# Kernel optimization log

Hardware: AMD Instinct MI355X
Metric: run time of the kernel (lower is better)

Reference implementation:

```python
import jax, jax.numpy as jnp
import numpy as np

N_NODES = 100000
N_EDGES = 1600000
IN_DIM = 256
HIDDEN = 128
N_CLASSES = 10


def setup_inputs() -> dict:
    key = jax.random.key(0)
    k1, k2, k3, k4 = jax.random.split(key, 4)
    x = jax.random.normal(k1, (N_NODES, IN_DIM), dtype=jnp.float32)
    edge_index = jax.random.randint(k2, (2, N_EDGES), 0, N_NODES, dtype=jnp.int64)
    # Glorot-ish init for weights
    W1 = jax.random.normal(k3, (IN_DIM, HIDDEN), dtype=jnp.float32) * (1.0 / np.sqrt(IN_DIM))
    b1 = jnp.zeros((HIDDEN,), dtype=jnp.float32)
    W2 = jax.random.normal(k4, (HIDDEN, N_CLASSES), dtype=jnp.float32) * (1.0 / np.sqrt(HIDDEN))
    b2 = jnp.zeros((N_CLASSES,), dtype=jnp.float32)
    return {"x": x, "edge_index": edge_index, "W1": W1, "b1": b1, "W2": W2, "b2": b2}


def _gcn_norm(edge_index, num_nodes):
    # PyG gcn_norm with add_self_loops=False, edge_weight=1:
    # deg over destination (col), norm = d^-1/2[src] * d^-1/2[dst]
    row, col = edge_index[0], edge_index[1]
    deg = jax.ops.segment_sum(jnp.ones((edge_index.shape[1],), jnp.float32), col,
                              num_segments=num_nodes)
    dinv = jnp.where(deg > 0, jax.lax.rsqrt(jnp.maximum(deg, 1.0)), 0.0)
    return dinv[row] * dinv[col]


def _gcn_conv(x, W, b, row, col, norm, num_nodes):
    h = x @ W                              # [N, out] dense transform
    msg = h[row] * norm[:, None]           # gather + scale, [E, out]
    out = jax.ops.segment_sum(msg, col, num_segments=num_nodes)  # scatter-add
    return out + b


def reference(x, edge_index, W1, b1, W2, b2):
    row, col = edge_index[0], edge_index[1]
    norm = _gcn_norm(edge_index, N_NODES)
    h = _gcn_conv(x, W1, b1, row, col, norm, N_NODES)
    h = jax.nn.relu(h)  # dropout is identity in eval mode
    out = _gcn_conv(h, W2, b2, row, col, norm, N_NODES)
    return out
```

## Files before the change

### kernel.cpp

```cpp
#include <hip/hip_runtime.h>
#include <hip/hip_fp16.h>

typedef _Float16 f16x8 __attribute__((ext_vector_type(8)));
typedef _Float16 f16x2 __attribute__((ext_vector_type(2)));
typedef float f32x4 __attribute__((ext_vector_type(4)));

#define NBUK_MAX 512
#define CHUNK 4096
#define BUKCAP 6144
#define WPAD 264
#define W1T_BLOCKS 64


__global__ __launch_bounds__(512) void k_fat1(const float* __restrict__ W1,
                                              __half* __restrict__ W1T,
                                              const int* __restrict__ row,
                                              const int* __restrict__ col,
                                              int* __restrict__ bcur,
                                              unsigned* __restrict__ pairs,
                                              int E, int nbuk) {
    __shared__ int hist[NBUK_MAX];
    __shared__ int scanA[NBUK_MAX];
    __shared__ int scanB[NBUK_MAX];
    __shared__ int cur[NBUK_MAX];
    __shared__ int gpos[NBUK_MAX];
    __shared__ unsigned staged[CHUNK];
    int tid = threadIdx.x;

    if (blockIdx.x < W1T_BLOCKS) {
        int idx = blockIdx.x * 512 + tid;
        int c = idx >> 8, k = idx & 255;
        W1T[(size_t)c * 256 + k] = __float2half(W1[(size_t)k * 128 + c]);
        return;
    }

    int bid = blockIdx.x - W1T_BLOCKS;
    int e0 = bid * CHUNK;
    int nv = E - e0; if (nv > CHUNK) nv = CHUNK;

    hist[tid] = 0;
    __syncthreads();
    if (nv == CHUNK) {
        const int4* c4 = (const int4*)(col + e0);
#pragma unroll
        for (int it = 0; it < 2; ++it) {
            int4 v = c4[tid + it * 512];
            atomicAdd(&hist[v.x >> 8], 1);
            atomicAdd(&hist[v.y >> 8], 1);
            atomicAdd(&hist[v.z >> 8], 1);
            atomicAdd(&hist[v.w >> 8], 1);
        }
    } else {
        for (int i = tid; i < nv; i += 512) atomicAdd(&hist[col[e0 + i] >> 8], 1);
    }
    __syncthreads();
    int hv = hist[tid];
    scanA[tid] = hv;
    __syncthreads();
    int* pa = scanA;
    int* pb = scanB;
    for (int off = 1; off < 512; off <<= 1) {
        pb[tid] = pa[tid] + ((tid >= off) ? pa[tid - off] : 0);
        __syncthreads();
        int* sw = pa; pa = pb; pb = sw;
    }
    int ex = pa[tid] - hv;
    __syncthreads();
    pb[tid] = ex;
    cur[tid] = ex;
    if (tid < nbuk && hv > 0) gpos[tid] = atomicAdd(&bcur[tid], hv);
    __syncthreads();
    int* excl = pb;
    if (nv == CHUNK) {
        const int4* c4 = (const int4*)(col + e0);
        const int4* r4 = (const int4*)(row + e0);
#pragma unroll
        for (int it = 0; it < 2; ++it) {
            int4 c = c4[tid + it * 512];
            int4 r = r4[tid + it * 512];
            int rk;
            rk = atomicAdd(&cur[c.x >> 8], 1); staged[rk] = ((unsigned)(c.x & 255) << 17) | (unsigned)r.x;
            rk = atomicAdd(&cur[c.y >> 8], 1); staged[rk] = ((unsigned)(c.y & 255) << 17) | (unsigned)r.y;
            rk = atomicAdd(&cur[c.z >> 8], 1); staged[rk] = ((unsigned)(c.z & 255) << 17) | (unsigned)r.z;
            rk = atomicAdd(&cur[c.w >> 8], 1); staged[rk] = ((unsigned)(c.w & 255) << 17) | (unsigned)r.w;
        }
    } else {
        for (int i = tid; i < nv; i += 512) {
            int c = col[e0 + i], r = row[e0 + i];
            int rk = atomicAdd(&cur[c >> 8], 1);
            staged[rk] = ((unsigned)(c & 255) << 17) | (unsigned)r;
        }
    }
    __syncthreads();
    int grp = tid >> 4, l16 = tid & 15;
    for (int b = grp; b < nbuk; b += 32) {
        int cnt = hist[b];
        if (cnt == 0) continue;
        int bs = excl[b];
        int gp = gpos[b];
        unsigned* dst = pairs + (size_t)b * BUKCAP;
        for (int l = l16; l < cnt; l += 16) {
            int d = gp + l;
            if (d < BUKCAP) dst[d] = staged[bs + l];
        }
    }
}


__global__ void k_bscan(const int* __restrict__ bcur, int* __restrict__ bbase, int nbuk) {
    __shared__ int s[512];
    int tid = threadIdx.x;
    int v = (tid < nbuk) ? bcur[tid] : 0;
    s[tid] = v;
    __syncthreads();
    for (int off = 1; off < 512; off <<= 1) {
        int tv = (tid >= off) ? s[tid - off] : 0;
        __syncthreads();
        s[tid] += tv;
        __syncthreads();
    }
    if (tid < nbuk) bbase[tid] = s[tid] - v;
}


__global__ __launch_bounds__(256) void k_csr2a(const unsigned* __restrict__ pairs,
                                               const int* __restrict__ bcur,
                                               const int* __restrict__ bbase,
                                               int* __restrict__ colptr,
                                               float* __restrict__ dinv,
                                               int N, int E) {
    __shared__ int fc[256];
    __shared__ int cp[256];
    __shared__ int tp[256];
    int b = blockIdx.x;
    int c0 = b << 8;
    int tid = threadIdx.x;
    fc[tid] = 0;
    __syncthreads();
    int cnt = bcur[b];
    if (cnt > BUKCAP) cnt = BUKCAP;
    int p0 = bbase[b];
    const unsigned* pbk = pairs + (size_t)b * BUKCAP;
    for (int i = tid; i < cnt; i += 256) {
        atomicAdd(&fc[pbk[i] >> 17], 1);
    }
    __syncthreads();
    int deg = fc[tid];
    cp[tid] = deg;
    __syncthreads();
    int* pa = cp;
    int* pb = tp;
    for (int off = 1; off < 256; off <<= 1) {
        pb[tid] = pa[tid] + ((tid >= off) ? pa[tid - off] : 0);
        __syncthreads();
        int* sw = pa; pa = pb; pb = sw;
    }
    int excl = pa[tid] - deg;
    if (c0 + tid < N) {
        colptr[c0 + tid] = p0 + excl;
        dinv[c0 + tid] = (deg > 0) ? rsqrtf((float)deg) : 0.0f;
    }
    if (b == 0 && tid == 0) colptr[N] = E;
}


#define SMEM_BYTES (128 * WPAD * 2)

__global__ __launch_bounds__(512, 4) void k_fat2(const unsigned* __restrict__ pairs,
                                                 const int* __restrict__ bcur,
                                                 const int* __restrict__ bbase,
                                                 const int* __restrict__ colptr,
                                                 int* __restrict__ srcs,
                                                 const float* __restrict__ x,
                                                 const __half* __restrict__ W1T,
                                                 const float* __restrict__ dinv,
                                                 __half* __restrict__ h,
                                                 int N, int nbuk) {
    __shared__ __align__(16) char smem[SMEM_BYTES];
    int tid = threadIdx.x;

    if (blockIdx.x < nbuk) {
        int* tp  = (int*)smem;
        int* fc  = tp + 256;
        int* loc = fc + 256;
        int b = blockIdx.x;
        int c0 = b << 8;
        int cnt = bcur[b];
        if (cnt > BUKCAP) cnt = BUKCAP;
        int p0 = bbase[b];
        if (tid < 256) {
            fc[tid] = 0;
            tp[tid] = (c0 + tid < N) ? (colptr[c0 + tid] - p0) : 0;
        }
        __syncthreads();
        const unsigned* pbk = pairs + (size_t)b * BUKCAP;
        for (int i = tid; i < cnt; i += 512) {
            unsigned v = pbk[i];
            int cl = (int)(v >> 17);
            int r = (int)(v & 0x1FFFFu);
            int off = tp[cl] + atomicAdd(&fc[cl], 1);
            if (off < BUKCAP) loc[off] = r;
            else srcs[p0 + off] = r;
        }
        __syncthreads();
        for (int i = tid; i < cnt; i += 512) srcs[p0 + i] = loc[i];
        return;
    }

    __half (*wt)[WPAD] = (__half(*)[WPAD])smem;
    int gb = blockIdx.x - nbuk;
    int w = tid >> 6, l = tid & 63;
    int r16 = l & 15, kg = l >> 4;
    int r0 = gb * 128;
    int rowi = r0 + w * 16 + r16;
    int rl = (rowi < N) ? rowi : 0;
    const float4* xp = (const float4*)x + (size_t)rl * 64 + kg * 2;

    float4 xr[8];
#pragma unroll
    for (int p = 0; p < 4; ++p) {
        xr[2 * p]     = xp[p * 8];
        xr[2 * p + 1] = xp[p * 8 + 1];
    }

#pragma unroll
    for (int it = 0; it < 8; ++it) {
        int idx = tid + it * 512;
        int c = idx >> 5, q = idx & 31;
        *(float4*)&wt[c][q * 8] = ((const float4*)W1T)[(size_t)c * 32 + q];
    }
    __syncthreads();

    f32x4 acc[8];
#pragma unroll
    for (int n = 0; n < 8; ++n) acc[n] = (f32x4){0.f, 0.f, 0.f, 0.f};

#pragma unroll
    for (int ks = 0; ks < 8; ++ks) {
        float4 c0 = xr[2 * (ks & 3)];
        float4 c1 = xr[2 * (ks & 3) + 1];
        if (ks < 4) {
            xr[2 * (ks & 3)]     = xp[(ks + 4) * 8];
            xr[2 * (ks & 3) + 1] = xp[(ks + 4) * 8 + 1];
        }
        f16x8 a;
        a[0] = (_Float16)c0.x; a[1] = (_Float16)c0.y;
        a[2] = (_Float16)c0.z; a[3] = (_Float16)c0.w;
        a[4] = (_Float16)c1.x; a[5] = (_Float16)c1.y;
        a[6] = (_Float16)c1.z; a[7] = (_Float16)c1.w;
        int kk = ks * 32;
#pragma unroll
        for (int n = 0; n < 8; ++n) {
            f16x8 b = *(const f16x8*)&wt[n * 16 + r16][kk + kg * 8];
            acc[n] = __builtin_amdgcn_mfma_f32_16x16x32_f16(a, b, acc[n], 0, 0, 0);
        }
    }

    float dn[4];
#pragma unroll
    for (int rr = 0; rr < 4; ++rr) {
        int r = r0 + w * 16 + kg * 4 + rr;
        dn[rr] = (r < N) ? dinv[r] : 0.f;
    }
#pragma unroll
    for (int n = 0; n < 8; ++n)
#pragma unroll
        for (int rr = 0; rr < 4; ++rr) {
            int r = r0 + w * 16 + kg * 4 + rr;
            if (r < N)
                h[(size_t)r * 128 + n * 16 + r16] = __float2half(dn[rr] * acc[n][rr]);
        }
}


#define LOAD8(sv, k, vv) { \
    int s0_ = __shfl(sv, (k) + 0), s1_ = __shfl(sv, (k) + 1); \
    int s2_ = __shfl(sv, (k) + 2), s3_ = __shfl(sv, (k) + 3); \
    int s4_ = __shfl(sv, (k) + 4), s5_ = __shfl(sv, (k) + 5); \
    int s6_ = __shfl(sv, (k) + 6), s7_ = __shfl(sv, (k) + 7); \
    vv[0] = hp[(size_t)s0_ * 64 + lane]; vv[1] = hp[(size_t)s1_ * 64 + lane]; \
    vv[2] = hp[(size_t)s2_ * 64 + lane]; vv[3] = hp[(size_t)s3_ * 64 + lane]; \
    vv[4] = hp[(size_t)s4_ * 64 + lane]; vv[5] = hp[(size_t)s5_ * 64 + lane]; \
    vv[6] = hp[(size_t)s6_ * 64 + lane]; vv[7] = hp[(size_t)s7_ * 64 + lane]; }

#define ACC8(vv, A0, A1) { \
    float2 f0_ = __half22float2(vv[0]), f1_ = __half22float2(vv[1]); \
    float2 f2_ = __half22float2(vv[2]), f3_ = __half22float2(vv[3]); \
    float2 f4_ = __half22float2(vv[4]), f5_ = __half22float2(vv[5]); \
    float2 f6_ = __half22float2(vv[6]), f7_ = __half22float2(vv[7]); \
    A0 += ((f0_.x + f1_.x) + (f2_.x + f3_.x)) + ((f4_.x + f5_.x) + (f6_.x + f7_.x)); \
    A1 += ((f0_.y + f1_.y) + (f2_.y + f3_.y)) + ((f4_.y + f5_.y) + (f6_.y + f7_.y)); }

__global__ __launch_bounds__(256) void k_agg1(const __half* __restrict__ h,
                                              const float* __restrict__ dinv,
                                              const int* __restrict__ colptr,
                                              const int* __restrict__ srcs,
                                              const float* __restrict__ b1,
                                              const float* __restrict__ W2,
                                              __half* __restrict__ t, int N) {
    __shared__ __half hs[64][136];
    __shared__ __half w2t[10][136];
    int tid = threadIdx.x;
    int wave = tid >> 6;
    int lane = tid & 63;

    for (int i = tid; i < 1280; i += 256) {
        int c = i >> 7, k = i & 127;
        w2t[c][k] = __float2half(W2[(size_t)k * 10 + c]);
    }

    const __half2* hp = (const __half2*)h;
    int nb0 = blockIdx.x * 64;
    float bb0 = b1[2 * lane], bb1 = b1[2 * lane + 1];

#pragma unroll 1
    for (int i = 0; i < 16; ++i) {
        int n = nb0 + wave * 16 + i;
        if (n >= N) break;
        int jb = colptr[n], je = colptr[n + 1];
        int len = je - jb;
        float a0 = 0.f, a1 = 0.f;
        for (int j0 = 0; j0 < len; j0 += 64) {
            int cnt = len - j0;
            if (cnt > 64) cnt = 64;
            int sv = (lane < cnt) ? srcs[jb + j0 + lane] : 0;
            int k = 0;
            for (; k + 8 <= cnt; k += 8) {
                __half2 va[8];
                LOAD8(sv, k, va);
                ACC8(va, a0, a1);
            }
            for (; k < cnt; ++k) {
                int s = __shfl(sv, k);
                float2 f = __half22float2(hp[(size_t)s * 64 + lane]);
                a0 += f.x; a1 += f.y;
            }
        }
        float dn = dinv[n];
        float v0 = dn * a0 + bb0;
        float v1 = dn * a1 + bb1;
        v0 = v0 > 0.f ? v0 : 0.f;
        v1 = v1 > 0.f ? v1 : 0.f;
        ((__half2*)&hs[wave * 16 + i][0])[lane] = __floats2half2_rn(v0, v1);
    }
    __syncthreads();

#pragma unroll
    for (int it = 0; it < 4; ++it) {
        int idx = tid + it * 256;
        int r = idx >> 4, c = idx & 15;
        int n = nb0 + r;
        if (n < N) {
            float s = 0.f;
            if (c < 10) {
                const f16x2* hr = (const f16x2*)&hs[r][0];
                const f16x2* wr = (const f16x2*)&w2t[c][0];
#pragma unroll
                for (int j = 0; j < 64; ++j)
                    s = __builtin_amdgcn_fdot2(hr[j], wr[j], s, false);
                s *= dinv[n];
            }
            t[(size_t)n * 16 + c] = __float2half(s);
        }
    }
}


__global__ __launch_bounds__(256) void k_agg2(const __half* __restrict__ t,
                                              const float* __restrict__ dinv,
                                              const int* __restrict__ colptr,
                                              const int* __restrict__ srcs,
                                              const float* __restrict__ b2,
                                              float* __restrict__ out, int N) {
    int g = threadIdx.x >> 4;
    int lane16 = threadIdx.x & 15;
    int wg = g & 3;
    int n = blockIdx.x * 16 + g;
    if (n >= N) return;
    int jb = colptr[n], je = colptr[n + 1];
    float a = 0.f;
    for (int j0 = jb; j0 < je; j0 += 16) {
        int cnt = je - j0;
        if (cnt > 16) cnt = 16;
        int sv = (lane16 < cnt) ? srcs[j0 + lane16] : 0;
        int k = 0;
        for (; k + 4 <= cnt; k += 4) {
            int s0 = __shfl(sv, wg * 16 + k + 0);
            int s1 = __shfl(sv, wg * 16 + k + 1);
            int s2 = __shfl(sv, wg * 16 + k + 2);
            int s3 = __shfl(sv, wg * 16 + k + 3);
            float x0 = __half2float(t[(size_t)s0 * 16 + lane16]);
            float x1 = __half2float(t[(size_t)s1 * 16 + lane16]);
            float x2 = __half2float(t[(size_t)s2 * 16 + lane16]);
            float x3 = __half2float(t[(size_t)s3 * 16 + lane16]);
            a += (x0 + x1) + (x2 + x3);
        }
        for (; k < cnt; ++k) {
            int s = __shfl(sv, wg * 16 + k);
            a += __half2float(t[(size_t)s * 16 + lane16]);
        }
    }
    if (lane16 < 10) out[(size_t)n * 10 + lane16] = dinv[n] * a + b2[lane16];
}


static inline size_t alignup(size_t x) { return (x + 255) & ~(size_t)255; }

extern "C" void kernel_launch(void* const* d_in, const int* in_sizes, int n_in,
                              void* d_out, int out_size, void* d_ws, size_t ws_size,
                              hipStream_t stream) {
    const float* x  = (const float*)d_in[0];
    const int*   ei = (const int*)d_in[1];
    const float* W1 = (const float*)d_in[2];
    const float* b1 = (const float*)d_in[3];
    const float* W2 = (const float*)d_in[4];
    const float* b2 = (const float*)d_in[5];

    int E = in_sizes[1] / 2;
    int N = in_sizes[0] / 256;
    const int* row = ei;
    const int* col = ei + E;
    int nbuk = (N + 255) >> 8;
    int nbE = (E + CHUNK - 1) / CHUNK;
    int nbG1 = (N + 127) / 128;

    char* ws = (char*)d_ws;
    size_t off = 0;
    int*      colptr = (int*)(ws + off);      off += alignup((size_t)(N + 1) * 4);
    float*    dinv   = (float*)(ws + off);    off += alignup((size_t)N * 4);
    int*      bbase  = (int*)(ws + off);      off += alignup((size_t)NBUK_MAX * 4);
    int*      bcur   = (int*)(ws + off);      off += alignup((size_t)NBUK_MAX * 4);
    int*      srcs   = (int*)(ws + off);      off += alignup((size_t)E * 4);
    unsigned* pairs  = (unsigned*)(ws + off); off += alignup((size_t)NBUK_MAX * BUKCAP * 4);
    __half*   W1T    = (__half*)(ws + off);   off += alignup((size_t)128 * 256 * 2);
    __half*   h      = (__half*)(ws + off);   off += alignup((size_t)N * 128 * 2);
    __half*   t      = (__half*)(ws + off);   off += alignup((size_t)N * 16 * 2);

    hipMemsetAsync(bcur, 0, (size_t)NBUK_MAX * 4, stream);

    k_fat1<<<W1T_BLOCKS + nbE, 512, 0, stream>>>(W1, W1T, row, col, bcur, pairs, E, nbuk);
    k_bscan<<<1, 512, 0, stream>>>(bcur, bbase, nbuk);
    k_csr2a<<<nbuk, 256, 0, stream>>>(pairs, bcur, bbase, colptr, dinv, N, E);
    k_fat2<<<nbuk + nbG1, 512, 0, stream>>>(pairs, bcur, bbase, colptr, srcs,
                                            x, W1T, dinv, h, N, nbuk);
    k_agg1<<<(N + 63) / 64, 256, 0, stream>>>(h, dinv, colptr, srcs, b1, W2, t, N);
    k_agg2<<<(N + 15) / 16, 256, 0, stream>>>(t, dinv, colptr, srcs, b2, (float*)d_out, N);
}
```

Before: 159.9 us.

## Fold bucket scan into CSR kernel, pad bucket counters, widen dot and gather loops

Removes the single-block bucket scan launch by having each k_csr2a block redundantly scan all bucket counts in shared memory, and derives each bucket's base from colptr in k_fat2. Bucket counters are padded to a 16-int stride to cut contention between neighbouring atomics. The layer-2 dot product now uses 16-byte vector loads, and the agg2 gather loop is unrolled to 8 loads. These save a launch and reduce memory latency stalls, at the cost of a redundant 512-entry scan in every csr2a block.

```diff
diff --git a/kernel.cpp b/kernel.cpp
--- a/kernel.cpp
+++ b/kernel.cpp
@@ -10,6 +10,7 @@
 #define BUKCAP 6144
 #define WPAD 264
 #define W1T_BLOCKS 64
+#define BSTR 16
 
 
 __global__ __launch_bounds__(512) void k_fat1(const float* __restrict__ W1,
@@ -68,7 +69,7 @@
     __syncthreads();
     pb[tid] = ex;
     cur[tid] = ex;
-    if (tid < nbuk && hv > 0) gpos[tid] = atomicAdd(&bcur[tid], hv);
+    if (tid < nbuk && hv > 0) gpos[tid] = atomicAdd(&bcur[tid * BSTR], hv);
     __syncthreads();
     int* excl = pb;
     if (nv == CHUNK) {
@@ -107,39 +108,42 @@
 }
 
 
-__global__ void k_bscan(const int* __restrict__ bcur, int* __restrict__ bbase, int nbuk) {
-    __shared__ int s[512];
-    int tid = threadIdx.x;
-    int v = (tid < nbuk) ? bcur[tid] : 0;
-    s[tid] = v;
-    __syncthreads();
-    for (int off = 1; off < 512; off <<= 1) {
-        int tv = (tid >= off) ? s[tid - off] : 0;
-        __syncthreads();
-        s[tid] += tv;
-        __syncthreads();
-    }
-    if (tid < nbuk) bbase[tid] = s[tid] - v;
-}
-
-
 __global__ __launch_bounds__(256) void k_csr2a(const unsigned* __restrict__ pairs,
                                                const int* __restrict__ bcur,
-                                               const int* __restrict__ bbase,
                                                int* __restrict__ colptr,
                                                float* __restrict__ dinv,
                                                int N, int E) {
     __shared__ int fc[256];
     __shared__ int cp[256];
     __shared__ int tp[256];
+    __shared__ int sA[NBUK_MAX];
+    __shared__ int sB[NBUK_MAX];
     int b = blockIdx.x;
     int c0 = b << 8;
     int tid = threadIdx.x;
     fc[tid] = 0;
-    __syncthreads();
-    int cnt = bcur[b];
-    if (cnt > BUKCAP) cnt = BUKCAP;
-    int p0 = bbase[b];
+#pragma unroll
+    for (int q = 0; q < 2; ++q) {
+        int i = tid + q * 256;
+        sA[i] = bcur[i * BSTR];
+    }
+    __syncthreads();
+    int* pa = sA;
+    int* pb = sB;
+    for (int off = 1; off < 512; off <<= 1) {
+#pragma unroll
+        for (int q = 0; q < 2; ++q) {
+            int i = tid + q * 256;
+            pb[i] = pa[i] + ((i >= off) ? pa[i - off] : 0);
+        }
+        __syncthreads();
+        int* sw = pa; pa = pb; pb = sw;
+    }
+    int cntb = bcur[b * BSTR];
+    int p0 = pa[b] - cntb;
+    int cnt = cntb > BUKCAP ? BUKCAP : cntb;
+    __syncthreads();
+
     const unsigned* pbk = pairs + (size_t)b * BUKCAP;
     for (int i = tid; i < cnt; i += 256) {
         atomicAdd(&fc[pbk[i] >> 17], 1);
@@ -148,8 +152,7 @@
     int deg = fc[tid];
     cp[tid] = deg;
     __syncthreads();
-    int* pa = cp;
-    int* pb = tp;
+    pa = cp; pb = tp;
     for (int off = 1; off < 256; off <<= 1) {
         pb[tid] = pa[tid] + ((tid >= off) ? pa[tid - off] : 0);
         __syncthreads();
@@ -168,7 +171,6 @@
 
 __global__ __launch_bounds__(512, 4) void k_fat2(const unsigned* __restrict__ pairs,
                                                  const int* __restrict__ bcur,
-                                                 const int* __restrict__ bbase,
                                                  const int* __restrict__ colptr,
                                                  int* __restrict__ srcs,
                                                  const float* __restrict__ x,
@@ -185,9 +187,9 @@
         int* loc = fc + 256;
         int b = blockIdx.x;
         int c0 = b << 8;
-        int cnt = bcur[b];
+        int cnt = bcur[b * BSTR];
         if (cnt > BUKCAP) cnt = BUKCAP;
-        int p0 = bbase[b];
+        int p0 = colptr[c0];
         if (tid < 256) {
             fc[tid] = 0;
             tp[tid] = (c0 + tid < N) ? (colptr[c0 + tid] - p0) : 0;
@@ -353,11 +355,18 @@
         if (n < N) {
             float s = 0.f;
             if (c < 10) {
-                const f16x2* hr = (const f16x2*)&hs[r][0];
-                const f16x2* wr = (const f16x2*)&w2t[c][0];
-#pragma unroll
-                for (int j = 0; j < 64; ++j)
-                    s = __builtin_amdgcn_fdot2(hr[j], wr[j], s, false);
+                const float4* hr4 = (const float4*)&hs[r][0];
+                const float4* wr4 = (const float4*)&w2t[c][0];
+#pragma unroll
+                for (int j = 0; j < 16; ++j) {
+                    union { float4 v; f16x2 h2[4]; } uh, uw;
+                    uh.v = hr4[j];
+                    uw.v = wr4[j];
+                    s = __builtin_amdgcn_fdot2(uh.h2[0], uw.h2[0], s, false);
+                    s = __builtin_amdgcn_fdot2(uh.h2[1], uw.h2[1], s, false);
+                    s = __builtin_amdgcn_fdot2(uh.h2[2], uw.h2[2], s, false);
+                    s = __builtin_amdgcn_fdot2(uh.h2[3], uw.h2[3], s, false);
+                }
                 s *= dinv[n];
             }
             t[(size_t)n * 16 + c] = __float2half(s);
@@ -384,16 +393,24 @@
         if (cnt > 16) cnt = 16;
         int sv = (lane16 < cnt) ? srcs[j0 + lane16] : 0;
         int k = 0;
-        for (; k + 4 <= cnt; k += 4) {
+        for (; k + 8 <= cnt; k += 8) {
             int s0 = __shfl(sv, wg * 16 + k + 0);
             int s1 = __shfl(sv, wg * 16 + k + 1);
             int s2 = __shfl(sv, wg * 16 + k + 2);
             int s3 = __shfl(sv, wg * 16 + k + 3);
+            int s4 = __shfl(sv, wg * 16 + k + 4);
+            int s5 = __shfl(sv, wg * 16 + k + 5);
+            int s6 = __shfl(sv, wg * 16 + k + 6);
+            int s7 = __shfl(sv, wg * 16 + k + 7);
             float x0 = __half2float(t[(size_t)s0 * 16 + lane16]);
             float x1 = __half2float(t[(size_t)s1 * 16 + lane16]);
             float x2 = __half2float(t[(size_t)s2 * 16 + lane16]);
             float x3 = __half2float(t[(size_t)s3 * 16 + lane16]);
-            a += (x0 + x1) + (x2 + x3);
+            float x4 = __half2float(t[(size_t)s4 * 16 + lane16]);
+            float x5 = __half2float(t[(size_t)s5 * 16 + lane16]);
+            float x6 = __half2float(t[(size_t)s6 * 16 + lane16]);
+            float x7 = __half2float(t[(size_t)s7 * 16 + lane16]);
+            a += ((x0 + x1) + (x2 + x3)) + ((x4 + x5) + (x6 + x7));
         }
         for (; k < cnt; ++k) {
             int s = __shfl(sv, wg * 16 + k);
@@ -428,20 +445,18 @@
     size_t off = 0;
     int*      colptr = (int*)(ws + off);      off += alignup((size_t)(N + 1) * 4);
     float*    dinv   = (float*)(ws + off);    off += alignup((size_t)N * 4);
-    int*      bbase  = (int*)(ws + off);      off += alignup((size_t)NBUK_MAX * 4);
-    int*      bcur   = (int*)(ws + off);      off += alignup((size_t)NBUK_MAX * 4);
+    int*      bcur   = (int*)(ws + off);      off += alignup((size_t)NBUK_MAX * BSTR * 4);
     int*      srcs   = (int*)(ws + off);      off += alignup((size_t)E * 4);
     unsigned* pairs  = (unsigned*)(ws + off); off += alignup((size_t)NBUK_MAX * BUKCAP * 4);
     __half*   W1T    = (__half*)(ws + off);   off += alignup((size_t)128 * 256 * 2);
     __half*   h      = (__half*)(ws + off);   off += alignup((size_t)N * 128 * 2);
     __half*   t      = (__half*)(ws + off);   off += alignup((size_t)N * 16 * 2);
 
-    hipMemsetAsync(bcur, 0, (size_t)NBUK_MAX * 4, stream);
+    hipMemsetAsync(bcur, 0, (size_t)NBUK_MAX * BSTR * 4, stream);
 
     k_fat1<<<W1T_BLOCKS + nbE, 512, 0, stream>>>(W1, W1T, row, col, bcur, pairs, E, nbuk);
-    k_bscan<<<1, 512, 0, stream>>>(bcur, bbase, nbuk);
-    k_csr2a<<<nbuk, 256, 0, stream>>>(pairs, bcur, bbase, colptr, dinv, N, E);
-    k_fat2<<<nbuk + nbG1, 512, 0, stream>>>(pairs, bcur, bbase, colptr, srcs,
+    k_csr2a<<<nbuk, 256, 0, stream>>>(pairs, bcur, colptr, dinv, N, E);
+    k_fat2<<<nbuk + nbG1, 512, 0, stream>>>(pairs, bcur, colptr, srcs,
                                             x, W1T, dinv, h, N, nbuk);
     k_agg1<<<(N + 63) / 64, 256, 0, stream>>>(h, dinv, colptr, srcs, b1, W2, t, N);
     k_agg2<<<(N + 15) / 16, 256, 0, stream>>>(t, dinv, colptr, srcs, b2, (float*)d_out, N);
```

Result: slower. 163.3 us (+2.1%).
